# Kernel tuning notes

Measured on AMD Instinct MI355X. Metric: run time of the kernel, lower is better.

The kernel has to match this reference:

```python
import jax, jax.numpy as jnp
import numpy as np

R_CUT = 10.0
ROUNDS = 1  # num_message_passing_rounds


def setup_inputs() -> dict:
    key = jax.random.key(0)
    N, DEG, S, NRBF, G = 10000, 16, 128, 20, 64
    E = N * DEG
    ks = jax.random.split(key, 16)
    w = lambda k, shp, fan: (jax.random.normal(k, shp, dtype=jnp.float32) / np.float32(np.sqrt(fan)))
    return {
        "edge_vector_diffs": jax.random.normal(ks[0], (E, 3), dtype=jnp.float32) * 3.0,
        "edge_lengths": jax.random.uniform(ks[1], (E,), dtype=jnp.float32) * 15.0,
        "node_from": jnp.repeat(jnp.arange(N), DEG),            # every node has DEG outgoing edges
        "node_graph_index": jax.random.randint(ks[2], (N,), 0, G),
        "num_graphs": G,
        "emb0": jax.random.normal(ks[3], (S,), dtype=jnp.float32) * 0.01,  # embedding.weight[0]
        "phi_w1": w(ks[4], (S, S), S), "phi_b1": jnp.zeros((S,), jnp.float32),
        "phi_w2": w(ks[5], (S, 3 * S), S), "phi_b2": jnp.zeros((3 * S,), jnp.float32),
        "filt_w": w(ks[6], (NRBF, 3 * S), NRBF), "filt_b": jnp.zeros((3 * S,), jnp.float32),
        "u_w": w(ks[7], (S, S), S), "v_w": w(ks[8], (S, S), S),
        "upd_w1": w(ks[9], (2 * S, S), 2 * S), "upd_b1": jnp.zeros((S,), jnp.float32),
        "upd_w2": w(ks[10], (S, 3 * S), S), "upd_b2": jnp.zeros((3 * S,), jnp.float32),
        "out_w1": w(ks[11], (S, S), S), "out_b1": jnp.zeros((S,), jnp.float32),
        "out_w2": w(ks[12], (S, 1), S), "out_b2": jnp.zeros((1,), jnp.float32),
    }


def reference(edge_vector_diffs, edge_lengths, node_from, node_graph_index, num_graphs,
              emb0, phi_w1, phi_b1, phi_w2, phi_b2, filt_w, filt_b, u_w, v_w,
              upd_w1, upd_b1, upd_w2, upd_b2, out_w1, out_b1, out_w2, out_b2):
    S = phi_w1.shape[0]
    N = node_graph_index.shape[0]
    NRBF = filt_w.shape[0]
    silu = jax.nn.silu
    seg = lambda v, n: jax.ops.segment_sum(v, node_from, num_segments=n)

    mask = (jnp.abs(edge_lengths) <= R_CUT).astype(jnp.float32)          # [E] nbr_mask
    r = jnp.linalg.norm(edge_vector_diffs, axis=1)                        # [E]
    r_safe = jnp.maximum(r, 1e-12)
    k = jnp.arange(1, NRBF + 1, dtype=jnp.float32)
    # PAINN sinc radial basis sin(k*pi*r/r_cut)/r, then linear -> [E, 3S]
    rbf = jnp.sin(k[None, :] * jnp.pi * r_safe[:, None] / R_CUT) / r_safe[:, None]
    cutoff = 0.5 * (jnp.cos(jnp.pi * r / R_CUT) + 1.0) * (r < R_CUT)      # cosine cutoff
    W = (rbf @ filt_w + filt_b) * cutoff[:, None]                          # [E, 3S]

    tile3 = jnp.arange(S) % 3  # xyzxyz... truncation pattern from .repeat(...)[: S]
    # scalar Frobenius norm of each node's masked neighbor-diff block
    frob = jnp.sqrt(seg(mask * r * r, N))                                  # [N]
    denom_e = frob[node_from]
    denom_e = jnp.where(denom_e > 0, denom_e, 1.0)
    normalized = edge_vector_diffs / denom_e[:, None]                      # [E, 3]
    norm_exp = normalized[:, tile3]                                        # [E, S]

    # state init: sum over dim 1 of embedding(zeros) == S * embedding.weight[0]
    state = jnp.broadcast_to(jnp.float32(S) * emb0, (N, S))
    state_vec = jnp.zeros((N, 3, S), jnp.float32)

    for _ in range(ROUNDS):
        # message block (nbrs_node_from == destination node, so sync update == original sequential loop)
        phi = silu(state[node_from] @ phi_w1 + phi_b1) @ phi_w2 + phi_b2   # [E, 3S]
        prod = phi * W
        m1, m2, m3 = prod[:, :S], prod[:, S:2 * S], prod[:, 2 * S:]
        vec_msg = state_vec[node_from] * m1[:, None, :] + (norm_exp * m3)[:, None, :]  # [E,3,S]
        state = seg(m2 * mask[:, None], N)                                 # [N, S]
        state_vec = seg(vec_msg * mask[:, None, None], N)                  # [N, 3, S]
        # update block
        U = jnp.einsum('nps,st->npt', state_vec, u_w)                      # [N,3,S]
        V = jnp.einsum('nps,st->npt', state_vec, v_w)
        UV = jnp.einsum('nps,nqs->npq', U, V)                              # [N,3,3]
        Vnorm = jnp.sqrt(jnp.sum(V * V, axis=1))                           # [N,S]
        a = silu(jnp.concatenate([Vnorm, state], axis=-1) @ upd_w1 + upd_b1) @ upd_w2 + upd_b2
        a_vv, a_sv, a_ss = a[:, :S], a[:, S:2 * S], a[:, 2 * S:]
        uv_tiled = jnp.sum(UV, axis=1)[:, tile3]                           # [N,S]
        state = a_ss + uv_tiled * a_sv
        state_vec = U * a_vv[:, None, :]

    graph_state = jax.ops.segment_sum(state, node_graph_index, num_segments=num_graphs)
    out = (silu(graph_state @ out_w1 + out_b1) @ out_w2 + out_b2).ravel()  # [num_graphs]
    return out
```

## Files before the change

### kernel.cpp

```cpp
#include <hip/hip_runtime.h>
#include <math.h>

#define NN   10000
#define DEG  16
#define SS   128
#define NRBF 20
#define GG   64
#define RC   10.0f
#define PI_F 3.14159265358979323846f
#define NB   4

__device__ __forceinline__ float silu_f(float x){
    return x / (1.0f + __expf(-x));
}

__global__ __launch_bounds__(128) void k_phi(
    const float* __restrict__ emb0,
    const float* __restrict__ w1, const float* __restrict__ b1,
    const float* __restrict__ w2, const float* __restrict__ b2,
    float* __restrict__ phiW){
    __shared__ float s0[SS];
    __shared__ float hL[SS];
    __shared__ float part[2][4];
    int t = threadIdx.x, bid = blockIdx.x;
    s0[t] = 128.0f * emb0[t];
    __syncthreads();
    float acc = 0.0f;
    #pragma unroll 8
    for (int s = 0; s < SS; s++)
        acc = fmaf(s0[s], w1[s*SS + t], acc);
    hL[t] = silu_f(acc + b1[t]);
    __syncthreads();
    int c0 = bid * 4;
    float4 wq = *((const float4*)(w2 + t*3*SS + c0));
    float h = hL[t];
    float p[4] = {h*wq.x, h*wq.y, h*wq.z, h*wq.w};
    int lane = t & 63, wid = t >> 6;
    #pragma unroll
    for (int j = 0; j < 4; j++){
        float v = p[j];
        for (int off = 32; off; off >>= 1) v += __shfl_down(v, off);
        if (lane == 0) part[wid][j] = v;
    }
    __syncthreads();
    if (t < 4) phiW[c0 + t] = b2[c0 + t] + part[0][t] + part[1][t];
}

__global__ __launch_bounds__(128) void k_node(
    const float* __restrict__ evd, const float* __restrict__ elen,
    const float* __restrict__ filt_w, const float* __restrict__ filt_b,
    const float* __restrict__ phiW,
    const float* __restrict__ u_w, const float* __restrict__ v_w,
    const float* __restrict__ upd_w1, const float* __restrict__ upd_b1,
    const float* __restrict__ upd_w2, const float* __restrict__ upd_b2,
    const int* __restrict__ ngi, float* __restrict__ gs){
    __shared__ float rS[NB*DEG];
    __shared__ float mcL[NB*DEG];
    __shared__ float frL[NB*DEG];
    __shared__ float eV[NB*DEG][3];
    __shared__ float rbfL[NB*DEG][NRBF];
    __shared__ float invD[NB];
    __shared__ __align__(16) float svT[SS][NB];
    __shared__ __align__(16) float xT[2*SS][NB];
    __shared__ __align__(16) float h2T[SS][NB];
    __shared__ float red[2][NB];
    __shared__ float dL[NB];
    int t  = threadIdx.x;
    int n0 = blockIdx.x * NB;

    if (t < NB*DEG){
        int e = n0*DEG + t;
        float x = evd[3*e+0], y = evd[3*e+1], z = evd[3*e+2];
        float r = sqrtf(x*x + y*y + z*z);
        float len  = elen[e];
        float mask = (fabsf(len) <= RC) ? 1.0f : 0.0f;
        float cut  = (r < RC) ? 0.5f*(cosf(PI_F*r*(1.0f/RC)) + 1.0f) : 0.0f;
        rS[t]  = fmaxf(r, 1e-12f);
        mcL[t] = mask * cut;
        frL[t] = mask * r * r;
        eV[t][0] = x; eV[t][1] = y; eV[t][2] = z;
    }
    __syncthreads();
    for (int idx = t; idx < NB*DEG*NRBF; idx += 128){
        int e = idx / NRBF, k = idx % NRBF;
        float rs = rS[e];
        rbfL[e][k] = sinf((float)(k+1) * (PI_F/RC) * rs) / rs;
    }
    if (t < NB){
        float s = 0.0f;
        for (int j = 0; j < DEG; j++) s += frL[t*DEG + j];
        float fbn = sqrtf(s);
        invD[t] = (fbn > 0.0f) ? 1.0f/fbn : 1.0f;
    }
    __syncthreads();

    {
        int gc1 = SS + t;
        int gc2 = 2*SS + t;
        float fw1[NRBF], fw2[NRBF];
        #pragma unroll
        for (int k = 0; k < NRBF; k++){
            fw1[k] = filt_w[k*(3*SS) + gc1];
            fw2[k] = filt_w[k*(3*SS) + gc2];
        }
        float fb1 = filt_b[gc1], fb2 = filt_b[gc2];
        float ph1 = phiW[gc1],   ph2 = phiW[gc2];
        int   s3  = t % 3;

        for (int b = 0; b < NB; b++){
            float iD = invD[b];
            float acc1 = 0.0f, acc2 = 0.0f;
            for (int e = 0; e < DEG; e++){
                int ee = b*DEG + e;
                float mc = mcL[ee];
                if (mc == 0.0f) continue;
                const float4* rv = (const float4*)(&rbfL[ee][0]);
                float4 r0 = rv[0], r1 = rv[1], r2 = rv[2], r3 = rv[3], r4 = rv[4];
                float rr[20] = {r0.x,r0.y,r0.z,r0.w, r1.x,r1.y,r1.z,r1.w,
                                r2.x,r2.y,r2.z,r2.w, r3.x,r3.y,r3.z,r3.w,
                                r4.x,r4.y,r4.z,r4.w};
                float w1v = fb1, w2v = fb2;
                #pragma unroll
                for (int k = 0; k < NRBF; k++){
                    w1v = fmaf(rr[k], fw1[k], w1v);
                    w2v = fmaf(rr[k], fw2[k], w2v);
                }
                acc1 = fmaf(ph1*mc, w1v, acc1);
                acc2 = fmaf(ph2*mc*eV[ee][s3]*iD, w2v, acc2);
            }
            svT[t][b]   = acc2;
            xT[SS+t][b] = acc1;
        }
    }
    __syncthreads();

    float accU[NB], accV[NB];
    #pragma unroll
    for (int b = 0; b < NB; b++){ accU[b]=0.f; accV[b]=0.f; }
    for (int s = 0; s < SS; s++){
        float wu = u_w[s*SS + t];
        float wv = v_w[s*SS + t];
        float4 s03 = *((const float4*)(&svT[s][0]));
        float svv[NB] = {s03.x,s03.y,s03.z,s03.w};
        #pragma unroll
        for (int b = 0; b < NB; b++){
            accU[b] = fmaf(svv[b], wu, accU[b]);
            accV[b] = fmaf(svv[b], wv, accV[b]);
        }
    }

    int lane = t & 63, wid = t >> 6;
    #pragma unroll
    for (int b = 0; b < NB; b++){
        float p = accU[b]*accV[b];
        for (int off = 32; off; off >>= 1) p += __shfl_down(p, off);
        if (lane == 0) red[wid][b] = p;
    }
    {
        float4 q0;
        q0.x = sqrtf(3.f*accV[0]*accV[0]); q0.y = sqrtf(3.f*accV[1]*accV[1]);
        q0.z = sqrtf(3.f*accV[2]*accV[2]); q0.w = sqrtf(3.f*accV[3]*accV[3]);
        ((float4*)(&xT[t][0]))[0] = q0;
    }
    __syncthreads();
    if (t < NB) dL[t] = red[0][t] + red[1][t];

    float accH[NB];
    #pragma unroll
    for (int b = 0; b < NB; b++) accH[b] = 0.f;
    for (int i = 0; i < 2*SS; i++){
        float w = upd_w1[i*SS + t];
        float4 x03 = *((const float4*)(&xT[i][0]));
        float xv[NB] = {x03.x,x03.y,x03.z,x03.w};
        #pragma unroll
        for (int b = 0; b < NB; b++) accH[b] = fmaf(xv[b], w, accH[b]);
    }
    float b1v = upd_b1[t];
    {
        float4 q0;
        q0.x = silu_f(accH[0]+b1v); q0.y = silu_f(accH[1]+b1v);
        q0.z = silu_f(accH[2]+b1v); q0.w = silu_f(accH[3]+b1v);
        ((float4*)(&h2T[t][0]))[0] = q0;
    }
    __syncthreads();

    float a1[NB], a2[NB];
    #pragma unroll
    for (int b = 0; b < NB; b++){ a1[b]=0.f; a2[b]=0.f; }
    for (int j = 0; j < SS; j++){
        float w1 = upd_w2[j*3*SS + SS   + t];
        float w2 = upd_w2[j*3*SS + 2*SS + t];
        float4 h03 = *((const float4*)(&h2T[j][0]));
        float hv[NB] = {h03.x,h03.y,h03.z,h03.w};
        #pragma unroll
        for (int b = 0; b < NB; b++){
            a1[b] = fmaf(hv[b], w1, a1[b]);
            a2[b] = fmaf(hv[b], w2, a2[b]);
        }
    }
    float bsv = upd_b2[SS+t], bss = upd_b2[2*SS+t];
    #pragma unroll
    for (int b = 0; b < NB; b++){
        float ns = (a2[b] + bss) + 3.0f*dL[b]*(a1[b] + bsv);
        int g = ngi[n0+b];
        atomicAdd(&gs[g*SS + t], ns);
    }
}

__global__ __launch_bounds__(128) void k_out(
    const float* __restrict__ gs,
    const float* __restrict__ w1, const float* __restrict__ b1,
    const float* __restrict__ w2, const float* __restrict__ b2,
    float* __restrict__ out){
    __shared__ float gsL[SS];
    __shared__ float red[2];
    int g = blockIdx.x, t = threadIdx.x;
    gsL[t] = gs[g*SS + t];
    __syncthreads();
    float acc = b1[t];
    #pragma unroll 4
    for (int s = 0; s < SS; s++) acc = fmaf(gsL[s], w1[s*SS + t], acc);
    float p = silu_f(acc) * w2[t];
    for (int off = 32; off; off >>= 1) p += __shfl_down(p, off);
    if ((t & 63) == 0) red[t >> 6] = p;
    __syncthreads();
    if (t == 0) out[g] = red[0] + red[1] + b2[0];
}

extern "C" void kernel_launch(void* const* d_in, const int* in_sizes, int n_in,
                              void* d_out, int out_size, void* d_ws, size_t ws_size,
                              hipStream_t stream) {
    const float* evd     = (const float*)d_in[0];
    const float* elen    = (const float*)d_in[1];
    const int*   ngi     = (const int*)  d_in[3];
    const float* emb0    = (const float*)d_in[5];
    const float* phi_w1  = (const float*)d_in[6];
    const float* phi_b1  = (const float*)d_in[7];
    const float* phi_w2  = (const float*)d_in[8];
    const float* phi_b2  = (const float*)d_in[9];
    const float* filt_w  = (const float*)d_in[10];
    const float* filt_b  = (const float*)d_in[11];
    const float* u_w     = (const float*)d_in[12];
    const float* v_w     = (const float*)d_in[13];
    const float* upd_w1  = (const float*)d_in[14];
    const float* upd_b1  = (const float*)d_in[15];
    const float* upd_w2  = (const float*)d_in[16];
    const float* upd_b2  = (const float*)d_in[17];
    const float* out_w1  = (const float*)d_in[18];
    const float* out_b1  = (const float*)d_in[19];
    const float* out_w2  = (const float*)d_in[20];
    const float* out_b2  = (const float*)d_in[21];

    float* ws    = (float*)d_ws;
    float* phiW  = ws;
    float* gs    = ws + 512;

    hipMemsetAsync(gs, 0, GG*SS*sizeof(float), stream);
    k_phi<<<96, 128, 0, stream>>>(emb0, phi_w1, phi_b1, phi_w2, phi_b2, phiW);
    k_node<<<NN/NB, 128, 0, stream>>>(evd, elen, filt_w, filt_b, phiW,
                                      u_w, v_w, upd_w1, upd_b1, upd_w2, upd_b2,
                                      ngi, gs);
    k_out<<<GG, 128, 0, stream>>>(gs, out_w1, out_b1, out_w2, out_b2, (float*)d_out);
}
```

Before: 172.8 us.

## Pre-reduce edge RBF sums per node before applying filter weights

Uses linearity of the filter projection: the mask*cutoff weighted (and edge-vector weighted) RBF values are first summed over the 16 edges of each node into a small shared table, including a column for the bias. Each output channel then does 20 FMAs per node instead of 16x20 per node. This removes most of the per-edge filter matmul work. It adds one extra shared-memory reduction pass and a barrier, and it changes the floating-point summation order.

```diff
diff --git a/kernel.cpp b/kernel.cpp
--- a/kernel.cpp
+++ b/kernel.cpp
@@ -60,6 +60,7 @@
     __shared__ float eV[NB*DEG][3];
     __shared__ float rbfL[NB*DEG][NRBF];
     __shared__ float invD[NB];
+    __shared__ float gsum[NB][4][NRBF+1];
     __shared__ __align__(16) float svT[SS][NB];
     __shared__ __align__(16) float xT[2*SS][NB];
     __shared__ __align__(16) float h2T[SS][NB];
@@ -94,6 +95,24 @@
     }
     __syncthreads();
 
+    for (int idx = t; idx < NB*4*(NRBF+1); idx += 128){
+        int n   = idx / (4*(NRBF+1));
+        int rem = idx % (4*(NRBF+1));
+        int q   = rem / (NRBF+1);
+        int k   = rem % (NRBF+1);
+        float s = 0.0f;
+        #pragma unroll
+        for (int e = 0; e < DEG; e++){
+            int ee = n*DEG + e;
+            float w = mcL[ee];
+            if (q > 0) w *= eV[ee][q-1];
+            float rb = (k < NRBF) ? rbfL[ee][k] : 1.0f;
+            s = fmaf(w, rb, s);
+        }
+        gsum[n][q][k] = s;
+    }
+    __syncthreads();
+
     {
         int gc1 = SS + t;
         int gc2 = 2*SS + t;
@@ -107,29 +126,17 @@
         float ph1 = phiW[gc1],   ph2 = phiW[gc2];
         int   s3  = t % 3;
 
+        #pragma unroll
         for (int b = 0; b < NB; b++){
-            float iD = invD[b];
-            float acc1 = 0.0f, acc2 = 0.0f;
-            for (int e = 0; e < DEG; e++){
-                int ee = b*DEG + e;
-                float mc = mcL[ee];
-                if (mc == 0.0f) continue;
-                const float4* rv = (const float4*)(&rbfL[ee][0]);
-                float4 r0 = rv[0], r1 = rv[1], r2 = rv[2], r3 = rv[3], r4 = rv[4];
-                float rr[20] = {r0.x,r0.y,r0.z,r0.w, r1.x,r1.y,r1.z,r1.w,
-                                r2.x,r2.y,r2.z,r2.w, r3.x,r3.y,r3.z,r3.w,
-                                r4.x,r4.y,r4.z,r4.w};
-                float w1v = fb1, w2v = fb2;
-                #pragma unroll
-                for (int k = 0; k < NRBF; k++){
-                    w1v = fmaf(rr[k], fw1[k], w1v);
-                    w2v = fmaf(rr[k], fw2[k], w2v);
-                }
-                acc1 = fmaf(ph1*mc, w1v, acc1);
-                acc2 = fmaf(ph2*mc*eV[ee][s3]*iD, w2v, acc2);
+            float a1 = fb1 * gsum[b][0][NRBF];
+            float a2 = fb2 * gsum[b][s3+1][NRBF];
+            #pragma unroll
+            for (int k = 0; k < NRBF; k++){
+                a1 = fmaf(gsum[b][0][k],    fw1[k], a1);
+                a2 = fmaf(gsum[b][s3+1][k], fw2[k], a2);
             }
-            svT[t][b]   = acc2;
-            xT[SS+t][b] = acc1;
+            svT[t][b]   = ph2 * invD[b] * a2;
+            xT[SS+t][b] = ph1 * a1;
         }
     }
     __syncthreads();
```

Result: no change. 174.1 us (+0.8%).

## Process eight nodes per block with 2x4 register tiles for node GEMVs

Applied to the files above, without the earlier changes.

Doubles the nodes handled per block and reworks the per-node matrix products so each thread computes a 2-node by 4-column register tile, loading weights as float4. Shared buffers are transposed to node-major, and the U·V reduction becomes a 32-lane shuffle within each thread group. This halves weight reads per node from global/L2 and raises arithmetic intensity, but halves the grid size (1250 blocks) and increases register and shared-memory use. Edge preprocessing now uses all 128 threads for 128 edges.

```diff
diff --git a/kernel.cpp b/kernel.cpp
--- a/kernel.cpp
+++ b/kernel.cpp
@@ -8,7 +8,7 @@
 #define GG   64
 #define RC   10.0f
 #define PI_F 3.14159265358979323846f
-#define NB   4
+#define NB   8
 
 __device__ __forceinline__ float silu_f(float x){
     return x / (1.0f + __expf(-x));
@@ -60,15 +60,18 @@
     __shared__ float eV[NB*DEG][3];
     __shared__ float rbfL[NB*DEG][NRBF];
     __shared__ float invD[NB];
-    __shared__ __align__(16) float svT[SS][NB];
-    __shared__ __align__(16) float xT[2*SS][NB];
-    __shared__ __align__(16) float h2T[SS][NB];
-    __shared__ float red[2][NB];
+    __shared__ __align__(16) float svT[NB][SS];
+    __shared__ __align__(16) float xT[NB][2*SS];
+    __shared__ __align__(16) float h2T[NB][SS];
     __shared__ float dL[NB];
+    __shared__ int   gL[NB];
     int t  = threadIdx.x;
+    int cq = t & 31;
+    int c0 = cq * 4;
+    int pr = t >> 5;
     int n0 = blockIdx.x * NB;
 
-    if (t < NB*DEG){
+    {
         int e = n0*DEG + t;
         float x = evd[3*e+0], y = evd[3*e+1], z = evd[3*e+2];
         float r = sqrtf(x*x + y*y + z*z);
@@ -80,6 +83,7 @@
         frL[t] = mask * r * r;
         eV[t][0] = x; eV[t][1] = y; eV[t][2] = z;
     }
+    if (t < NB) gL[t] = ngi[n0 + t];
     __syncthreads();
     for (int idx = t; idx < NB*DEG*NRBF; idx += 128){
         int e = idx / NRBF, k = idx % NRBF;
@@ -128,82 +132,121 @@
                 acc1 = fmaf(ph1*mc, w1v, acc1);
                 acc2 = fmaf(ph2*mc*eV[ee][s3]*iD, w2v, acc2);
             }
-            svT[t][b]   = acc2;
-            xT[SS+t][b] = acc1;
+            svT[b][t]      = acc2;
+            xT[b][SS + t]  = acc1;
         }
     }
     __syncthreads();
 
-    float accU[NB], accV[NB];
-    #pragma unroll
-    for (int b = 0; b < NB; b++){ accU[b]=0.f; accV[b]=0.f; }
+    float accU[2][4], accV[2][4];
+    #pragma unroll
+    for (int b = 0; b < 2; b++)
+        #pragma unroll
+        for (int j = 0; j < 4; j++){ accU[b][j]=0.f; accV[b][j]=0.f; }
     for (int s = 0; s < SS; s++){
-        float wu = u_w[s*SS + t];
-        float wv = v_w[s*SS + t];
-        float4 s03 = *((const float4*)(&svT[s][0]));
-        float svv[NB] = {s03.x,s03.y,s03.z,s03.w};
-        #pragma unroll
-        for (int b = 0; b < NB; b++){
-            accU[b] = fmaf(svv[b], wu, accU[b]);
-            accV[b] = fmaf(svv[b], wv, accV[b]);
+        float4 wu = *((const float4*)(u_w + s*SS + c0));
+        float4 wv = *((const float4*)(v_w + s*SS + c0));
+        float wua[4] = {wu.x,wu.y,wu.z,wu.w};
+        float wva[4] = {wv.x,wv.y,wv.z,wv.w};
+        float sn[2] = { svT[2*pr+0][s], svT[2*pr+1][s] };
+        #pragma unroll
+        for (int b = 0; b < 2; b++)
+            #pragma unroll
+            for (int j = 0; j < 4; j++){
+                accU[b][j] = fmaf(sn[b], wua[j], accU[b][j]);
+                accV[b][j] = fmaf(sn[b], wva[j], accV[b][j]);
+            }
+    }
+    #pragma unroll
+    for (int b = 0; b < 2; b++){
+        float p = accU[b][0]*accV[b][0] + accU[b][1]*accV[b][1]
+                + accU[b][2]*accV[b][2] + accU[b][3]*accV[b][3];
+        #pragma unroll
+        for (int off = 16; off; off >>= 1) p += __shfl_down(p, off, 32);
+        if (cq == 0) dL[2*pr + b] = p;
+    }
+    #pragma unroll
+    for (int b = 0; b < 2; b++){
+        float4 q;
+        q.x = sqrtf(3.f*accV[b][0]*accV[b][0]);
+        q.y = sqrtf(3.f*accV[b][1]*accV[b][1]);
+        q.z = sqrtf(3.f*accV[b][2]*accV[b][2]);
+        q.w = sqrtf(3.f*accV[b][3]*accV[b][3]);
+        *((float4*)(&xT[2*pr+b][c0])) = q;
+    }
+    __syncthreads();
+
+    float accH[2][4];
+    #pragma unroll
+    for (int b = 0; b < 2; b++)
+        #pragma unroll
+        for (int j = 0; j < 4; j++) accH[b][j] = 0.f;
+    for (int i = 0; i < 2*SS; i++){
+        float4 w = *((const float4*)(upd_w1 + i*SS + c0));
+        float wa[4] = {w.x,w.y,w.z,w.w};
+        float xv[2] = { xT[2*pr+0][i], xT[2*pr+1][i] };
+        #pragma unroll
+        for (int b = 0; b < 2; b++)
+            #pragma unroll
+            for (int j = 0; j < 4; j++)
+                accH[b][j] = fmaf(xv[b], wa[j], accH[b][j]);
+    }
+    {
+        float4 b1q = *((const float4*)(upd_b1 + c0));
+        float b1a[4] = {b1q.x,b1q.y,b1q.z,b1q.w};
+        #pragma unroll
+        for (int b = 0; b < 2; b++){
+            float4 q;
+            q.x = silu_f(accH[b][0] + b1a[0]);
+            q.y = silu_f(accH[b][1] + b1a[1]);
+            q.z = silu_f(accH[b][2] + b1a[2]);
+            q.w = silu_f(accH[b][3] + b1a[3]);
+            *((float4*)(&h2T[2*pr+b][c0])) = q;
         }
     }
-
-    int lane = t & 63, wid = t >> 6;
-    #pragma unroll
-    for (int b = 0; b < NB; b++){
-        float p = accU[b]*accV[b];
-        for (int off = 32; off; off >>= 1) p += __shfl_down(p, off);
-        if (lane == 0) red[wid][b] = p;
-    }
+    __syncthreads();
+
+    float a1[2][4], a2[2][4];
+    #pragma unroll
+    for (int b = 0; b < 2; b++)
+        #pragma unroll
+        for (int j = 0; j < 4; j++){ a1[b][j]=0.f; a2[b][j]=0.f; }
+    for (int s = 0; s < SS; s++){
+        float4 wa4 = *((const float4*)(upd_w2 + s*3*SS + SS   + c0));
+        float4 wb4 = *((const float4*)(upd_w2 + s*3*SS + 2*SS + c0));
+        float waa[4] = {wa4.x,wa4.y,wa4.z,wa4.w};
+        float wba[4] = {wb4.x,wb4.y,wb4.z,wb4.w};
+        float hv[2] = { h2T[2*pr+0][s], h2T[2*pr+1][s] };
+        #pragma unroll
+        for (int b = 0; b < 2; b++)
+            #pragma unroll
+            for (int j = 0; j < 4; j++){
+                a1[b][j] = fmaf(hv[b], waa[j], a1[b][j]);
+                a2[b][j] = fmaf(hv[b], wba[j], a2[b][j]);
+            }
+    }
+    __syncthreads();
+
     {
-        float4 q0;
-        q0.x = sqrtf(3.f*accV[0]*accV[0]); q0.y = sqrtf(3.f*accV[1]*accV[1]);
-        q0.z = sqrtf(3.f*accV[2]*accV[2]); q0.w = sqrtf(3.f*accV[3]*accV[3]);
-        ((float4*)(&xT[t][0]))[0] = q0;
-    }
-    __syncthreads();
-    if (t < NB) dL[t] = red[0][t] + red[1][t];
-
-    float accH[NB];
-    #pragma unroll
-    for (int b = 0; b < NB; b++) accH[b] = 0.f;
-    for (int i = 0; i < 2*SS; i++){
-        float w = upd_w1[i*SS + t];
-        float4 x03 = *((const float4*)(&xT[i][0]));
-        float xv[NB] = {x03.x,x03.y,x03.z,x03.w};
-        #pragma unroll
-        for (int b = 0; b < NB; b++) accH[b] = fmaf(xv[b], w, accH[b]);
-    }
-    float b1v = upd_b1[t];
-    {
-        float4 q0;
-        q0.x = silu_f(accH[0]+b1v); q0.y = silu_f(accH[1]+b1v);
-        q0.z = silu_f(accH[2]+b1v); q0.w = silu_f(accH[3]+b1v);
-        ((float4*)(&h2T[t][0]))[0] = q0;
-    }
-    __syncthreads();
-
-    float a1[NB], a2[NB];
-    #pragma unroll
-    for (int b = 0; b < NB; b++){ a1[b]=0.f; a2[b]=0.f; }
-    for (int j = 0; j < SS; j++){
-        float w1 = upd_w2[j*3*SS + SS   + t];
-        float w2 = upd_w2[j*3*SS + 2*SS + t];
-        float4 h03 = *((const float4*)(&h2T[j][0]));
-        float hv[NB] = {h03.x,h03.y,h03.z,h03.w};
-        #pragma unroll
-        for (int b = 0; b < NB; b++){
-            a1[b] = fmaf(hv[b], w1, a1[b]);
-            a2[b] = fmaf(hv[b], w2, a2[b]);
+        float4 bsvq = *((const float4*)(upd_b2 + SS   + c0));
+        float4 bssq = *((const float4*)(upd_b2 + 2*SS + c0));
+        float bsva[4] = {bsvq.x,bsvq.y,bsvq.z,bsvq.w};
+        float bssa[4] = {bssq.x,bssq.y,bssq.z,bssq.w};
+        #pragma unroll
+        for (int b = 0; b < 2; b++){
+            float d3 = 3.0f * dL[2*pr + b];
+            float4 q;
+            q.x = (a2[b][0] + bssa[0]) + d3*(a1[b][0] + bsva[0]);
+            q.y = (a2[b][1] + bssa[1]) + d3*(a1[b][1] + bsva[1]);
+            q.z = (a2[b][2] + bssa[2]) + d3*(a1[b][2] + bsva[2]);
+            q.w = (a2[b][3] + bssa[3]) + d3*(a1[b][3] + bsva[3]);
+            *((float4*)(&h2T[2*pr+b][c0])) = q;
         }
     }
-    float bsv = upd_b2[SS+t], bss = upd_b2[2*SS+t];
-    #pragma unroll
-    for (int b = 0; b < NB; b++){
-        float ns = (a2[b] + bss) + 3.0f*dL[b]*(a1[b] + bsv);
-        int g = ngi[n0+b];
-        atomicAdd(&gs[g*SS + t], ns);
+    __syncthreads();
+    #pragma unroll
+    for (int n = 0; n < NB; n++){
+        atomicAdd(&gs[gL[n]*SS + t], h2T[n][t]);
     }
 }
 
```

Result: slower. 199.9 us (+15.7%).

## Split k_node reductions across two thread halves with 256-thread blocks

Applied to the files above, without the earlier changes.

The node kernel now launches 256 threads per block instead of 128. The filter stage splits the 4 nodes between the two halves, and each matvec stage (U/V, update MLP layers) splits its reduction dimension between them. Partial sums go through shared memory and the first half combines them. This doubles the threads working on each 4-node block to raise latency hiding and parallelism, at the cost of extra shared memory, extra barriers and half the threads idling in the combine steps.

```diff
diff --git a/kernel.cpp b/kernel.cpp
--- a/kernel.cpp
+++ b/kernel.cpp
@@ -9,6 +9,7 @@
 #define RC   10.0f
 #define PI_F 3.14159265358979323846f
 #define NB   4
+#define TPB  256
 
 __device__ __forceinline__ float silu_f(float x){
     return x / (1.0f + __expf(-x));
@@ -46,7 +47,7 @@
     if (t < 4) phiW[c0 + t] = b2[c0 + t] + part[0][t] + part[1][t];
 }
 
-__global__ __launch_bounds__(128) void k_node(
+__global__ __launch_bounds__(256) void k_node(
     const float* __restrict__ evd, const float* __restrict__ elen,
     const float* __restrict__ filt_w, const float* __restrict__ filt_b,
     const float* __restrict__ phiW,
@@ -63,9 +64,13 @@
     __shared__ __align__(16) float svT[SS][NB];
     __shared__ __align__(16) float xT[2*SS][NB];
     __shared__ __align__(16) float h2T[SS][NB];
+    __shared__ float pA[2][NB][SS];
+    __shared__ float pB[2][NB][SS];
     __shared__ float red[2][NB];
     __shared__ float dL[NB];
     int t  = threadIdx.x;
+    int ch = t & 127;
+    int kk = t >> 7;
     int n0 = blockIdx.x * NB;
 
     if (t < NB*DEG){
@@ -81,7 +86,7 @@
         eV[t][0] = x; eV[t][1] = y; eV[t][2] = z;
     }
     __syncthreads();
-    for (int idx = t; idx < NB*DEG*NRBF; idx += 128){
+    for (int idx = t; idx < NB*DEG*NRBF; idx += TPB){
         int e = idx / NRBF, k = idx % NRBF;
         float rs = rS[e];
         rbfL[e][k] = sinf((float)(k+1) * (PI_F/RC) * rs) / rs;
@@ -95,8 +100,8 @@
     __syncthreads();
 
     {
-        int gc1 = SS + t;
-        int gc2 = 2*SS + t;
+        int gc1 = SS + ch;
+        int gc2 = 2*SS + ch;
         float fw1[NRBF], fw2[NRBF];
         #pragma unroll
         for (int k = 0; k < NRBF; k++){
@@ -105,9 +110,11 @@
         }
         float fb1 = filt_b[gc1], fb2 = filt_b[gc2];
         float ph1 = phiW[gc1],   ph2 = phiW[gc2];
-        int   s3  = t % 3;
-
-        for (int b = 0; b < NB; b++){
+        int   s3  = ch % 3;
+
+        #pragma unroll
+        for (int bb = 0; bb < 2; bb++){
+            int b = 2*kk + bb;
             float iD = invD[b];
             float acc1 = 0.0f, acc2 = 0.0f;
             for (int e = 0; e < DEG; e++){
@@ -128,82 +135,117 @@
                 acc1 = fmaf(ph1*mc, w1v, acc1);
                 acc2 = fmaf(ph2*mc*eV[ee][s3]*iD, w2v, acc2);
             }
-            svT[t][b]   = acc2;
-            xT[SS+t][b] = acc1;
-        }
-    }
-    __syncthreads();
-
-    float accU[NB], accV[NB];
-    #pragma unroll
-    for (int b = 0; b < NB; b++){ accU[b]=0.f; accV[b]=0.f; }
-    for (int s = 0; s < SS; s++){
-        float wu = u_w[s*SS + t];
-        float wv = v_w[s*SS + t];
-        float4 s03 = *((const float4*)(&svT[s][0]));
-        float svv[NB] = {s03.x,s03.y,s03.z,s03.w};
-        #pragma unroll
-        for (int b = 0; b < NB; b++){
-            accU[b] = fmaf(svv[b], wu, accU[b]);
-            accV[b] = fmaf(svv[b], wv, accV[b]);
-        }
-    }
-
-    int lane = t & 63, wid = t >> 6;
-    #pragma unroll
-    for (int b = 0; b < NB; b++){
-        float p = accU[b]*accV[b];
-        for (int off = 32; off; off >>= 1) p += __shfl_down(p, off);
-        if (lane == 0) red[wid][b] = p;
-    }
+            svT[ch][b]      = acc2;
+            xT[SS + ch][b]  = acc1;
+        }
+    }
+    __syncthreads();
+
     {
+        float accU[NB], accV[NB];
+        #pragma unroll
+        for (int b = 0; b < NB; b++){ accU[b]=0.f; accV[b]=0.f; }
+        int sBeg = 64*kk;
+        for (int s = sBeg; s < sBeg+64; s++){
+            float wu = u_w[s*SS + ch];
+            float wv = v_w[s*SS + ch];
+            float4 s03 = *((const float4*)(&svT[s][0]));
+            float svv[NB] = {s03.x,s03.y,s03.z,s03.w};
+            #pragma unroll
+            for (int b = 0; b < NB; b++){
+                accU[b] = fmaf(svv[b], wu, accU[b]);
+                accV[b] = fmaf(svv[b], wv, accV[b]);
+            }
+        }
+        #pragma unroll
+        for (int b = 0; b < NB; b++){
+            pA[kk][b][ch] = accU[b];
+            pB[kk][b][ch] = accV[b];
+        }
+    }
+    __syncthreads();
+    if (kk == 0){
+        float U[NB], V[NB];
+        #pragma unroll
+        for (int b = 0; b < NB; b++){
+            U[b] = pA[0][b][ch] + pA[1][b][ch];
+            V[b] = pB[0][b][ch] + pB[1][b][ch];
+        }
+        int lane = t & 63, wid = t >> 6;
+        #pragma unroll
+        for (int b = 0; b < NB; b++){
+            float p = U[b]*V[b];
+            for (int off = 32; off; off >>= 1) p += __shfl_down(p, off);
+            if (lane == 0) red[wid][b] = p;
+        }
         float4 q0;
-        q0.x = sqrtf(3.f*accV[0]*accV[0]); q0.y = sqrtf(3.f*accV[1]*accV[1]);
-        q0.z = sqrtf(3.f*accV[2]*accV[2]); q0.w = sqrtf(3.f*accV[3]*accV[3]);
-        ((float4*)(&xT[t][0]))[0] = q0;
+        q0.x = sqrtf(3.f*V[0]*V[0]); q0.y = sqrtf(3.f*V[1]*V[1]);
+        q0.z = sqrtf(3.f*V[2]*V[2]); q0.w = sqrtf(3.f*V[3]*V[3]);
+        ((float4*)(&xT[ch][0]))[0] = q0;
     }
     __syncthreads();
     if (t < NB) dL[t] = red[0][t] + red[1][t];
 
-    float accH[NB];
-    #pragma unroll
-    for (int b = 0; b < NB; b++) accH[b] = 0.f;
-    for (int i = 0; i < 2*SS; i++){
-        float w = upd_w1[i*SS + t];
-        float4 x03 = *((const float4*)(&xT[i][0]));
-        float xv[NB] = {x03.x,x03.y,x03.z,x03.w};
-        #pragma unroll
-        for (int b = 0; b < NB; b++) accH[b] = fmaf(xv[b], w, accH[b]);
-    }
-    float b1v = upd_b1[t];
     {
+        float accH[NB];
+        #pragma unroll
+        for (int b = 0; b < NB; b++) accH[b] = 0.f;
+        int iBeg = 128*kk;
+        for (int i = iBeg; i < iBeg+128; i++){
+            float w = upd_w1[i*SS + ch];
+            float4 x03 = *((const float4*)(&xT[i][0]));
+            float xv[NB] = {x03.x,x03.y,x03.z,x03.w};
+            #pragma unroll
+            for (int b = 0; b < NB; b++) accH[b] = fmaf(xv[b], w, accH[b]);
+        }
+        #pragma unroll
+        for (int b = 0; b < NB; b++) pA[kk][b][ch] = accH[b];
+    }
+    __syncthreads();
+    if (kk == 0){
+        float b1v = upd_b1[ch];
         float4 q0;
-        q0.x = silu_f(accH[0]+b1v); q0.y = silu_f(accH[1]+b1v);
-        q0.z = silu_f(accH[2]+b1v); q0.w = silu_f(accH[3]+b1v);
-        ((float4*)(&h2T[t][0]))[0] = q0;
-    }
-    __syncthreads();
-
-    float a1[NB], a2[NB];
-    #pragma unroll
-    for (int b = 0; b < NB; b++){ a1[b]=0.f; a2[b]=0.f; }
-    for (int j = 0; j < SS; j++){
-        float w1 = upd_w2[j*3*SS + SS   + t];
-        float w2 = upd_w2[j*3*SS + 2*SS + t];
-        float4 h03 = *((const float4*)(&h2T[j][0]));
-        float hv[NB] = {h03.x,h03.y,h03.z,h03.w};
-        #pragma unroll
-        for (int b = 0; b < NB; b++){
-            a1[b] = fmaf(hv[b], w1, a1[b]);
-            a2[b] = fmaf(hv[b], w2, a2[b]);
-        }
-    }
-    float bsv = upd_b2[SS+t], bss = upd_b2[2*SS+t];
-    #pragma unroll
-    for (int b = 0; b < NB; b++){
-        float ns = (a2[b] + bss) + 3.0f*dL[b]*(a1[b] + bsv);
-        int g = ngi[n0+b];
-        atomicAdd(&gs[g*SS + t], ns);
+        q0.x = silu_f(pA[0][0][ch] + pA[1][0][ch] + b1v);
+        q0.y = silu_f(pA[0][1][ch] + pA[1][1][ch] + b1v);
+        q0.z = silu_f(pA[0][2][ch] + pA[1][2][ch] + b1v);
+        q0.w = silu_f(pA[0][3][ch] + pA[1][3][ch] + b1v);
+        ((float4*)(&h2T[ch][0]))[0] = q0;
+    }
+    __syncthreads();
+
+    {
+        float a1[NB], a2[NB];
+        #pragma unroll
+        for (int b = 0; b < NB; b++){ a1[b]=0.f; a2[b]=0.f; }
+        int jBeg = 64*kk;
+        for (int j = jBeg; j < jBeg+64; j++){
+            float w1 = upd_w2[j*3*SS + SS   + ch];
+            float w2 = upd_w2[j*3*SS + 2*SS + ch];
+            float4 h03 = *((const float4*)(&h2T[j][0]));
+            float hv[NB] = {h03.x,h03.y,h03.z,h03.w};
+            #pragma unroll
+            for (int b = 0; b < NB; b++){
+                a1[b] = fmaf(hv[b], w1, a1[b]);
+                a2[b] = fmaf(hv[b], w2, a2[b]);
+            }
+        }
+        #pragma unroll
+        for (int b = 0; b < NB; b++){
+            pA[kk][b][ch] = a1[b];
+            pB[kk][b][ch] = a2[b];
+        }
+    }
+    __syncthreads();
+    if (kk == 0){
+        float bsv = upd_b2[SS+ch], bss = upd_b2[2*SS+ch];
+        #pragma unroll
+        for (int b = 0; b < NB; b++){
+            float A1 = pA[0][b][ch] + pA[1][b][ch];
+            float A2 = pB[0][b][ch] + pB[1][b][ch];
+            float ns = (A2 + bss) + 3.0f*dL[b]*(A1 + bsv);
+            int g = ngi[n0+b];
+            atomicAdd(&gs[g*SS + ch], ns);
+        }
     }
 }
 
@@ -257,7 +299,7 @@
 
     hipMemsetAsync(gs, 0, GG*SS*sizeof(float), stream);
     k_phi<<<96, 128, 0, stream>>>(emb0, phi_w1, phi_b1, phi_w2, phi_b2, phiW);
-    k_node<<<NN/NB, 128, 0, stream>>>(evd, elen, filt_w, filt_b, phiW,
+    k_node<<<NN/NB, TPB, 0, stream>>>(evd, elen, filt_w, filt_b, phiW,
                                       u_w, v_w, upd_w1, upd_b1, upd_w2, upd_b2,
                                       ngi, gs);
     k_out<<<GG, 128, 0, stream>>>(gs, out_w1, out_b1, out_w2, out_b2, (float*)d_out);
```

After: 208.1 us. +20.4%, slower.
